# Kernel tuning notes

Measured on AMD Instinct MI355X. Metric: run time of the kernel, lower is better.

The kernel has to match this reference:

```python
import jax, jax.numpy as jnp
import numpy as np

N, K, F, A = 20000, 32, 256, 128
BN_EPS = 1e-3  # Keras BatchNormalization default epsilon


def setup_inputs() -> dict:
    key = jax.random.key(0)
    k1, k2, k3, k4 = jax.random.split(key, 4)
    self_feats = jax.random.normal(k1, (N, F), dtype=jnp.float32)
    neigh_feats = jax.random.normal(k2, (N, K, F), dtype=jnp.float32)
    W_shared = jax.random.normal(k3, (F, A), dtype=jnp.float32) * (1.0 / np.sqrt(F))
    b_shared = jnp.zeros((A,), dtype=jnp.float32)
    gamma = jnp.ones((A,), dtype=jnp.float32)
    beta = jnp.zeros((A,), dtype=jnp.float32)
    W_out = jax.random.normal(k4, (2 * A, 1), dtype=jnp.float32) * (1.0 / np.sqrt(2 * A))
    b_out = jnp.zeros((1,), dtype=jnp.float32)
    return {"self_feats": self_feats, "neigh_feats": neigh_feats,
            "W_shared": W_shared, "b_shared": b_shared,
            "gamma": gamma, "beta": beta, "W_out": W_out, "b_out": b_out}


def _bn_train(x, gamma, beta):
    # BatchNorm in training mode: batch statistics over leading axis
    mean = jnp.mean(x, axis=0, keepdims=True)
    var = jnp.var(x, axis=0, keepdims=True)
    return (x - mean) * jax.lax.rsqrt(var + BN_EPS) * gamma + beta


def reference(self_feats, neigh_feats, W_shared, b_shared, gamma, beta, W_out, b_out):
    # shared Dense + BN on self features: [N, A]
    s = _bn_train(self_feats @ W_shared + b_shared, gamma, beta)
    # shared Dense on neighbor features, BN over flattened [N*K, A] batch
    n = neigh_feats.reshape(-1, F) @ W_shared + b_shared  # [N*K, A]
    n = _bn_train(n, gamma, beta).reshape(neigh_feats.shape[0], neigh_feats.shape[1], -1)  # [N, K, A]
    # broadcast self feats over neighbors and concat: [N, K, 2A]
    s_b = jnp.broadcast_to(s[:, None, :], n.shape)
    concat = jnp.concatenate([s_b, n], axis=2)
    # attention logits: Dense(2A -> 1), activation, softmax over neighbors
    logits = concat @ W_out + b_out  # [N, K, 1]
    logits = jax.nn.relu(logits)
    coeff = jax.nn.softmax(jnp.squeeze(logits, axis=2), axis=-1)  # [N, K]
    return coeff[:, :, None]  # [N, K, 1]
```

## Files before the change

kernel.cpp:

```cpp
#include <hip/hip_runtime.h>
#include <cstdint>
#include <cstddef>


typedef __attribute__((ext_vector_type(8))) short short8;
typedef __attribute__((ext_vector_type(4))) float float4v;

__device__ __forceinline__ unsigned short f2bf(float f) {
  union { float f; unsigned u; } v; v.f = f;
  unsigned r = v.u + 0x7FFFu + ((v.u >> 16) & 1u);
  return (unsigned short)(r >> 16);
}

__global__ __launch_bounds__(256) void transpose_w(const float* __restrict__ W,
                                                   unsigned short* __restrict__ Wt) {
  const int n = blockIdx.x;
  const int k = threadIdx.x;
  Wt[n * 256 + k] = f2bf(W[k * 128 + n]);
}

#define BM 128
#define APAD 40

__global__ __launch_bounds__(256) void stats_gemm(
    const float* __restrict__ X, int R, int nTiles,
    const unsigned short* __restrict__ Wt, float* __restrict__ partials) {
  __shared__ __align__(16) unsigned short As[BM * APAD];
  __shared__ __align__(16) unsigned short Bs[128 * APAD];
  __shared__ float csum[128];
  __shared__ float csq[128];

  const int tid  = threadIdx.x;
  const int lane = tid & 63;
  const int wv   = tid >> 6;
  const int waveM = wv >> 1;
  const int waveN = wv & 1;
  const int quad  = lane >> 4;
  const int l16   = lane & 15;

  float runsum = 0.f, runsq = 0.f;

  for (int t = blockIdx.x; t < nTiles; t += gridDim.x) {
    const int row0 = t * BM;
    float4v acc[4][4];
#pragma unroll
    for (int rb = 0; rb < 4; ++rb)
#pragma unroll
      for (int cb = 0; cb < 4; ++cb)
        acc[rb][cb] = (float4v){0.f, 0.f, 0.f, 0.f};

    for (int kc = 0; kc < 8; ++kc) {
      __syncthreads();
#pragma unroll
      for (int it = 0; it < 4; ++it) {
        int idx = it * 256 + tid;
        int r = idx >> 3, j = idx & 7;
        float4 v = make_float4(0.f, 0.f, 0.f, 0.f);
        int gr = row0 + r;
        if (gr < R) v = *(const float4*)(X + (size_t)gr * 256 + kc * 32 + j * 4);
        uint2 p;
        p.x = (unsigned)f2bf(v.x) | ((unsigned)f2bf(v.y) << 16);
        p.y = (unsigned)f2bf(v.z) | ((unsigned)f2bf(v.w) << 16);
        *(uint2*)&As[r * APAD + j * 4] = p;
      }
#pragma unroll
      for (int it = 0; it < 4; ++it) {
        int idx = it * 256 + tid;
        int n = idx >> 3, j = idx & 7;
        *(uint2*)&Bs[n * APAD + j * 4] =
            *(const uint2*)(Wt + n * 256 + kc * 32 + j * 4);
      }
      __syncthreads();

      short8 a[4], b[4];
#pragma unroll
      for (int rb = 0; rb < 4; ++rb)
        a[rb] = *(const short8*)&As[(waveM * 64 + rb * 16 + l16) * APAD + quad * 8];
#pragma unroll
      for (int cb = 0; cb < 4; ++cb)
        b[cb] = *(const short8*)&Bs[(waveN * 64 + cb * 16 + l16) * APAD + quad * 8];
#pragma unroll
      for (int rb = 0; rb < 4; ++rb)
#pragma unroll
        for (int cb = 0; cb < 4; ++cb)
          acc[rb][cb] = __builtin_amdgcn_mfma_f32_16x16x32_bf16(
              a[rb], b[cb], acc[rb][cb], 0, 0, 0);
    }

    __syncthreads();
    float ps[4], pq[4];
#pragma unroll
    for (int cb = 0; cb < 4; ++cb) {
      float s = 0.f, q = 0.f;
#pragma unroll
      for (int rb = 0; rb < 4; ++rb) {
#pragma unroll
        for (int rg = 0; rg < 4; ++rg) {
          int grow = row0 + waveM * 64 + rb * 16 + quad * 4 + rg;
          float x = acc[rb][cb][rg];
          x = (grow < R) ? x : 0.f;
          s += x;
          q += x * x;
        }
      }
      s += __shfl_xor(s, 16); s += __shfl_xor(s, 32);
      q += __shfl_xor(q, 16); q += __shfl_xor(q, 32);
      ps[cb] = s; pq[cb] = q;
    }
    if (waveM == 0 && quad == 0) {
#pragma unroll
      for (int cb = 0; cb < 4; ++cb) {
        int col = waveN * 64 + cb * 16 + l16;
        csum[col] = ps[cb];
        csq[col]  = pq[cb];
      }
    }
    __syncthreads();
    if (waveM == 1 && quad == 0) {
#pragma unroll
      for (int cb = 0; cb < 4; ++cb) {
        int col = waveN * 64 + cb * 16 + l16;
        csum[col] += ps[cb];
        csq[col]  += pq[cb];
      }
    }
    __syncthreads();
    if (tid < 128) runsum += csum[tid];
    else           runsq  += csq[tid - 128];
  }
  partials[blockIdx.x * 256 + tid] = (tid < 128) ? runsum : runsq;
}

__global__ __launch_bounds__(256) void reduce_partials(
    const float* __restrict__ ps, int ns, const float* __restrict__ pn, int nn,
    float* __restrict__ stats) {
  __shared__ float buf[256];
  const int c = blockIdx.x;
  const int tid = threadIdx.x;
  float a = 0.f;
  for (int g = tid; g < ns; g += 256) a += ps[(size_t)g * 256 + c];
  buf[tid] = a;
  __syncthreads();
  for (int s = 128; s > 0; s >>= 1) {
    if (tid < s) buf[tid] += buf[tid + s];
    __syncthreads();
  }
  if (tid == 0) stats[c] = buf[0];
  float b = 0.f;
  for (int g = tid; g < nn; g += 256) b += pn[(size_t)g * 256 + c];
  __syncthreads();
  buf[tid] = b;
  __syncthreads();
  for (int s = 128; s > 0; s >>= 1) {
    if (tid < s) buf[tid] += buf[tid + s];
    __syncthreads();
  }
  if (tid == 0) stats[256 + c] = buf[0];
}

__global__ __launch_bounds__(256) void setup_kernel(
    const float* __restrict__ stats, const float* __restrict__ W,
    const float* __restrict__ gamma, const float* __restrict__ beta,
    const float* __restrict__ Wout, const float* __restrict__ bout,
    float* __restrict__ v1, float* __restrict__ v2, float* __restrict__ Cout) {
  __shared__ float g1[128], g2[128], carr[128];
  const int tid = threadIdx.x;
  if (tid < 128) {
    const float invNs = 1.f / 20000.f, invNn = 1.f / 640000.f;
    float ms = stats[tid] * invNs;
    float vs = stats[128 + tid] * invNs - ms * ms;
    float is = rsqrtf(vs + 1e-3f);
    float mn = stats[256 + tid] * invNn;
    float vn = stats[384 + tid] * invNn - mn * mn;
    float in_ = rsqrtf(vn + 1e-3f);
    float w1 = Wout[tid], w2 = Wout[128 + tid];
    float G1 = is * gamma[tid] * w1;
    float G2 = in_ * gamma[tid] * w2;
    g1[tid] = G1;
    g2[tid] = G2;
    carr[tid] = beta[tid] * (w1 + w2) - ms * G1 - mn * G2;
  }
  __syncthreads();
  float s1 = 0.f, s2 = 0.f;
  const float* wr = W + tid * 128;
  for (int a = 0; a < 128; ++a) {
    float w = wr[a];
    s1 += w * g1[a];
    s2 += w * g2[a];
  }
  v1[tid] = s1;
  v2[tid] = s2;
  if (tid == 0) {
    float c = bout[0];
    for (int a = 0; a < 128; ++a) c += carr[a];
    Cout[0] = c;
  }
}

__global__ __launch_bounds__(256) void attn_final(
    const float* __restrict__ self, const float* __restrict__ neigh,
    const float* __restrict__ v1, const float* __restrict__ v2,
    const float* __restrict__ Cptr, float* __restrict__ out) {
  const int lane = threadIdx.x & 63;
  const int wv = threadIdx.x >> 6;
  const int i = blockIdx.x * 4 + wv;
  const float C = Cptr[0];
  const float4 w1v = *(const float4*)(v1 + lane * 4);
  const float4 w2v = *(const float4*)(v2 + lane * 4);

  float4 sv = *(const float4*)(self + (size_t)i * 256 + lane * 4);
  float sd = fmaf(sv.x, w1v.x, fmaf(sv.y, w1v.y, fmaf(sv.z, w1v.z, sv.w * w1v.w)));
#pragma unroll
  for (int m = 32; m >= 1; m >>= 1) sd += __shfl_xor(sd, m);

  const float4* np = (const float4*)(neigh + (size_t)i * 8192);
  float ml = 0.f;
#pragma unroll 4
  for (int k = 0; k < 32; ++k) {
    float4 nv = np[k * 64 + lane];
    float nd = fmaf(nv.x, w2v.x, fmaf(nv.y, w2v.y, fmaf(nv.z, w2v.z, nv.w * w2v.w)));
#pragma unroll
    for (int m = 32; m >= 1; m >>= 1) nd += __shfl_xor(nd, m);
    if ((lane & 31) == k) ml = nd;
  }
  float logit = fmaxf(ml + sd + C, 0.f);
  float mx = logit;
#pragma unroll
  for (int m = 16; m >= 1; m >>= 1) mx = fmaxf(mx, __shfl_xor(mx, m));
  float e = __expf(logit - mx);
  float ssum = e;
#pragma unroll
  for (int m = 16; m >= 1; m >>= 1) ssum += __shfl_xor(ssum, m);
  if (lane < 32) out[(size_t)i * 32 + lane] = e / ssum;
}

extern "C" void kernel_launch(void* const* d_in, const int* in_sizes, int n_in,
                              void* d_out, int out_size, void* d_ws, size_t ws_size,
                              hipStream_t stream) {
  const float* self  = (const float*)d_in[0];
  const float* neigh = (const float*)d_in[1];
  const float* W     = (const float*)d_in[2];
  const float* gamma = (const float*)d_in[4];
  const float* beta  = (const float*)d_in[5];
  const float* Wout  = (const float*)d_in[6];
  const float* bout  = (const float*)d_in[7];
  float* out = (float*)d_out;

  char* ws = (char*)d_ws;
  unsigned short* Wt = (unsigned short*)ws;
  float* part_s = (float*)(ws + 65536);
  float* part_n = part_s + 157 * 256;
  float* stats  = part_n + 1024 * 256;
  float* v1     = stats + 512;
  float* v2     = v1 + 256;
  float* Cc     = v2 + 256;

  hipLaunchKernelGGL(transpose_w, dim3(128), dim3(256), 0, stream, W, Wt);
  hipLaunchKernelGGL(stats_gemm, dim3(157), dim3(256), 0, stream,
                     self, 20000, 157, Wt, part_s);
  hipLaunchKernelGGL(stats_gemm, dim3(1024), dim3(256), 0, stream,
                     neigh, 640000, 5000, Wt, part_n);
  hipLaunchKernelGGL(reduce_partials, dim3(256), dim3(256), 0, stream,
                     part_s, 157, part_n, 1024, stats);
  hipLaunchKernelGGL(setup_kernel, dim3(1), dim3(256), 0, stream,
                     stats, W, gamma, beta, Wout, bout, v1, v2, Cc);
  hipLaunchKernelGGL(attn_final, dim3(5000), dim3(256), 0, stream,
                     self, neigh, v1, v2, Cc, out);
}
```

Baseline: 1.083 ms.

## Materialize bf16 projected features in GEMM and reuse them in attention pass

The stats GEMM now writes its projected outputs as bf16 to workspace, and the final attention kernel reads these compact 128-wide projections instead of re-reading the raw 256-wide fp32 neighbor features. The setup kernel no longer folds the BN/output weights back through W; it only emits per-channel scales. This is meant to cut the second full pass over the large neighbor tensor. In exchange it adds a scattered 2-byte store per element to the GEMM epilogue and uses bf16-rounded values for the logits.

```diff
diff --git a/kernel.cpp b/kernel.cpp
--- a/kernel.cpp
+++ b/kernel.cpp
@@ -10,6 +10,9 @@
   union { float f; unsigned u; } v; v.f = f;
   unsigned r = v.u + 0x7FFFu + ((v.u >> 16) & 1u);
   return (unsigned short)(r >> 16);
+}
+__device__ __forceinline__ float bfu(unsigned v) {
+  union { unsigned u; float f; } t; t.u = v << 16; return t.f;
 }
 
 __global__ __launch_bounds__(256) void transpose_w(const float* __restrict__ W,
@@ -24,7 +27,9 @@
 
 __global__ __launch_bounds__(256) void stats_gemm(
     const float* __restrict__ X, int R, int nTiles,
-    const unsigned short* __restrict__ Wt, float* __restrict__ partials) {
+    const unsigned short* __restrict__ Wt,
+    unsigned short* __restrict__ U,
+    float* __restrict__ partials) {
   __shared__ __align__(16) unsigned short As[BM * APAD];
   __shared__ __align__(16) unsigned short Bs[128 * APAD];
   __shared__ float csum[128];
@@ -91,6 +96,7 @@
     float ps[4], pq[4];
 #pragma unroll
     for (int cb = 0; cb < 4; ++cb) {
+      const int col = waveN * 64 + cb * 16 + l16;
       float s = 0.f, q = 0.f;
 #pragma unroll
       for (int rb = 0; rb < 4; ++rb) {
@@ -98,9 +104,11 @@
         for (int rg = 0; rg < 4; ++rg) {
           int grow = row0 + waveM * 64 + rb * 16 + quad * 4 + rg;
           float x = acc[rb][cb][rg];
-          x = (grow < R) ? x : 0.f;
-          s += x;
-          q += x * x;
+          if (grow < R) {
+            U[(size_t)grow * 128 + col] = f2bf(x);
+            s += x;
+            q += x * x;
+          }
         }
       }
       s += __shfl_xor(s, 16); s += __shfl_xor(s, 32);
@@ -158,38 +166,27 @@
   if (tid == 0) stats[256 + c] = buf[0];
 }
 
-__global__ __launch_bounds__(256) void setup_kernel(
-    const float* __restrict__ stats, const float* __restrict__ W,
+__global__ __launch_bounds__(128) void setup_kernel(
+    const float* __restrict__ stats,
     const float* __restrict__ gamma, const float* __restrict__ beta,
     const float* __restrict__ Wout, const float* __restrict__ bout,
-    float* __restrict__ v1, float* __restrict__ v2, float* __restrict__ Cout) {
-  __shared__ float g1[128], g2[128], carr[128];
+    float* __restrict__ G1, float* __restrict__ G2, float* __restrict__ Cout) {
+  __shared__ float carr[128];
   const int tid = threadIdx.x;
-  if (tid < 128) {
-    const float invNs = 1.f / 20000.f, invNn = 1.f / 640000.f;
-    float ms = stats[tid] * invNs;
-    float vs = stats[128 + tid] * invNs - ms * ms;
-    float is = rsqrtf(vs + 1e-3f);
-    float mn = stats[256 + tid] * invNn;
-    float vn = stats[384 + tid] * invNn - mn * mn;
-    float in_ = rsqrtf(vn + 1e-3f);
-    float w1 = Wout[tid], w2 = Wout[128 + tid];
-    float G1 = is * gamma[tid] * w1;
-    float G2 = in_ * gamma[tid] * w2;
-    g1[tid] = G1;
-    g2[tid] = G2;
-    carr[tid] = beta[tid] * (w1 + w2) - ms * G1 - mn * G2;
-  }
-  __syncthreads();
-  float s1 = 0.f, s2 = 0.f;
-  const float* wr = W + tid * 128;
-  for (int a = 0; a < 128; ++a) {
-    float w = wr[a];
-    s1 += w * g1[a];
-    s2 += w * g2[a];
-  }
-  v1[tid] = s1;
-  v2[tid] = s2;
+  const float invNs = 1.f / 20000.f, invNn = 1.f / 640000.f;
+  float ms = stats[tid] * invNs;
+  float vs = stats[128 + tid] * invNs - ms * ms;
+  float is = rsqrtf(vs + 1e-3f);
+  float mn = stats[256 + tid] * invNn;
+  float vn = stats[384 + tid] * invNn - mn * mn;
+  float in_ = rsqrtf(vn + 1e-3f);
+  float w1 = Wout[tid], w2 = Wout[128 + tid];
+  float g1 = is * gamma[tid] * w1;
+  float g2 = in_ * gamma[tid] * w2;
+  G1[tid] = g1;
+  G2[tid] = g2;
+  carr[tid] = beta[tid] * (w1 + w2) - ms * g1 - mn * g2;
+  __syncthreads();
   if (tid == 0) {
     float c = bout[0];
     for (int a = 0; a < 128; ++a) c += carr[a];
@@ -198,30 +195,46 @@
 }
 
 __global__ __launch_bounds__(256) void attn_final(
-    const float* __restrict__ self, const float* __restrict__ neigh,
-    const float* __restrict__ v1, const float* __restrict__ v2,
+    const unsigned short* __restrict__ Us,
+    const unsigned short* __restrict__ Un,
+    const float* __restrict__ G1, const float* __restrict__ G2,
     const float* __restrict__ Cptr, float* __restrict__ out) {
   const int lane = threadIdx.x & 63;
   const int wv = threadIdx.x >> 6;
   const int i = blockIdx.x * 4 + wv;
+  const int l16 = lane & 15;
+  const int l32 = lane & 31;
+  const int quarter = lane >> 4;
   const float C = Cptr[0];
-  const float4 w1v = *(const float4*)(v1 + lane * 4);
-  const float4 w2v = *(const float4*)(v2 + lane * 4);
-
-  float4 sv = *(const float4*)(self + (size_t)i * 256 + lane * 4);
-  float sd = fmaf(sv.x, w1v.x, fmaf(sv.y, w1v.y, fmaf(sv.z, w1v.z, sv.w * w1v.w)));
+
+  unsigned su = *(const unsigned*)(Us + (size_t)i * 128 + lane * 2);
+  float2 g1p = *(const float2*)(G1 + lane * 2);
+  float sd = fmaf(g1p.x, bfu(su), g1p.y * bfu(su >> 16));
 #pragma unroll
   for (int m = 32; m >= 1; m >>= 1) sd += __shfl_xor(sd, m);
 
-  const float4* np = (const float4*)(neigh + (size_t)i * 8192);
+  const float4 ga = *(const float4*)(G2 + l16 * 8);
+  const float4 gb = *(const float4*)(G2 + l16 * 8 + 4);
+  const unsigned short* un = Un + (size_t)i * 4096;
   float ml = 0.f;
-#pragma unroll 4
-  for (int k = 0; k < 32; ++k) {
-    float4 nv = np[k * 64 + lane];
-    float nd = fmaf(nv.x, w2v.x, fmaf(nv.y, w2v.y, fmaf(nv.z, w2v.z, nv.w * w2v.w)));
-#pragma unroll
-    for (int m = 32; m >= 1; m >>= 1) nd += __shfl_xor(nd, m);
-    if ((lane & 31) == k) ml = nd;
+#pragma unroll
+  for (int j = 0; j < 8; ++j) {
+    const int nb = j * 4 + quarter;
+    uint4 q = *(const uint4*)(un + nb * 128 + l16 * 8);
+    float p;
+    p = fmaf(ga.x, bfu(q.x), ga.y * bfu(q.x >> 16));
+    p = fmaf(ga.z, bfu(q.y), p); p = fmaf(ga.w, bfu(q.y >> 16), p);
+    p = fmaf(gb.x, bfu(q.z), p); p = fmaf(gb.y, bfu(q.z >> 16), p);
+    p = fmaf(gb.z, bfu(q.w), p); p = fmaf(gb.w, bfu(q.w >> 16), p);
+#pragma unroll
+    for (int m = 1; m <= 8; m <<= 1) p += __shfl_xor(p, m);
+    float s16 = __shfl_xor(p, 16);
+    float s32 = __shfl_xor(p, 32);
+    float s48 = __shfl_xor(s16, 32);
+    if ((l32 >> 2) == j) {
+      int x = (l32 & 3) ^ quarter;
+      ml = (x == 0) ? p : (x == 1) ? s16 : (x == 2) ? s32 : s48;
+    }
   }
   float logit = fmaxf(ml + sd + C, 0.f);
   float mx = logit;
@@ -248,22 +261,24 @@
 
   char* ws = (char*)d_ws;
   unsigned short* Wt = (unsigned short*)ws;
-  float* part_s = (float*)(ws + 65536);
+  unsigned short* Us = (unsigned short*)(ws + (1 << 16));
+  unsigned short* Un = Us + (size_t)20000 * 128;
+  float* part_s = (float*)(Un + (size_t)640000 * 128);
   float* part_n = part_s + 157 * 256;
   float* stats  = part_n + 1024 * 256;
-  float* v1     = stats + 512;
-  float* v2     = v1 + 256;
-  float* Cc     = v2 + 256;
+  float* G1     = stats + 512;
+  float* G2     = G1 + 128;
+  float* Cc     = G2 + 128;
 
   hipLaunchKernelGGL(transpose_w, dim3(128), dim3(256), 0, stream, W, Wt);
   hipLaunchKernelGGL(stats_gemm, dim3(157), dim3(256), 0, stream,
-                     self, 20000, 157, Wt, part_s);
+                     self, 20000, 157, Wt, Us, part_s);
   hipLaunchKernelGGL(stats_gemm, dim3(1024), dim3(256), 0, stream,
-                     neigh, 640000, 5000, Wt, part_n);
+                     neigh, 640000, 5000, Wt, Un, part_n);
   hipLaunchKernelGGL(reduce_partials, dim3(256), dim3(256), 0, stream,
                      part_s, 157, part_n, 1024, stats);
-  hipLaunchKernelGGL(setup_kernel, dim3(1), dim3(256), 0, stream,
-                     stats, W, gamma, beta, Wout, bout, v1, v2, Cc);
+  hipLaunchKernelGGL(setup_kernel, dim3(1), dim3(128), 0, stream,
+                     stats, gamma, beta, Wout, bout, G1, G2, Cc);
   hipLaunchKernelGGL(attn_final, dim3(5000), dim3(256), 0, stream,
-                     self, neigh, v1, v2, Cc, out);
-}
+                     Us, Un, G1, G2, Cc, out);
+}
```

Measured after the change: 1.033 ms. 4.6% less time.
